# Performance work log

Hardware: AMD Instinct MI355X
Metric: run time of the kernel (lower is better)

The kernel has to match this reference:

```python
import jax, jax.numpy as jnp
import numpy as np

N_EXPERTS = 8
D_MODEL = 1024
D_FF = 4096
BATCH = 4
SEQ = 4096


def setup_inputs() -> dict:
    key = jax.random.key(0)
    k1, k2, k3, k4 = jax.random.split(key, 4)
    hidden_states = jax.random.normal(k1, (BATCH, SEQ, D_MODEL), dtype=jnp.float32)
    expert_indices = jax.random.randint(k2, (BATCH, SEQ), 0, N_EXPERTS, dtype=jnp.int64)
    # Expert MLP params, scaled like standard init
    W1 = jax.random.normal(k3, (N_EXPERTS, D_MODEL, D_FF), dtype=jnp.float32) / np.sqrt(D_MODEL)
    b1 = jnp.zeros((N_EXPERTS, D_FF), dtype=jnp.float32)
    W2 = jax.random.normal(k4, (N_EXPERTS, D_FF, D_MODEL), dtype=jnp.float32) / np.sqrt(D_FF)
    b2 = jnp.zeros((N_EXPERTS, D_MODEL), dtype=jnp.float32)
    return {"hidden_states": hidden_states, "expert_indices": expert_indices,
            "W1": W1, "b1": b1, "W2": W2, "b2": b2}


def reference(hidden_states, expert_indices, W1, b1, W2, b2):
    B, S, D = hidden_states.shape
    flat = hidden_states.reshape(B * S, D)          # [T, D]
    idx = expert_indices.reshape(-1)                 # [T]
    out = jnp.zeros_like(flat)
    # Fixed small loop over experts (structurally distinct weights).
    # jit-friendly: each expert runs over all tokens, output masked per token.
    for e in range(W1.shape[0]):
        h = jax.nn.gelu(flat @ W1[e] + b1[e])        # [T, F]
        y = h @ W2[e] + b2[e]                        # [T, D]
        out = out + jnp.where((idx == e)[:, None], y, jnp.float32(0.0))
    return out.reshape(B, S, D)
```

## Files before the change

kernel.cpp:

```cpp
#include <hip/hip_runtime.h>

#define T_TOK 16384
#define DMODEL 1024
#define DFF 4096
#define NEXP 8
#define BM 128
#define BN 128
#define BK 32
#define LDA 40
#define LDB 40
#define TPAD (T_TOK + NEXP * BM)

#define SEG8 256
#define TP256 (T_TOK + NEXP * SEG8)
#define BM2 256
#define BN2 128
#define BK2 64

typedef __bf16 bf16x8 __attribute__((ext_vector_type(8)));
typedef float f32x4 __attribute__((ext_vector_type(4)));

#define GLOAD16(gp, lp) __builtin_amdgcn_global_load_lds( \
    (const __attribute__((address_space(1))) void*)(gp), \
    (__attribute__((address_space(3))) void*)(lp), 16, 0, 0)

#define MFMA16(a, b, c) __builtin_amdgcn_mfma_f32_16x16x32_bf16(a, b, c, 0, 0, 0)

__device__ __forceinline__ float gelu_f(float x) {
  float u = 0.7978845608028654f * (x + 0.044715f * x * x * x);
  float e = __expf(2.0f * u);
  float th = 1.0f - 2.0f / (e + 1.0f);
  return 0.5f * x * (1.0f + th);
}

__global__ void k_init(int* counts, int* cursors, int* bucket, int n) {
  int i = blockIdx.x * blockDim.x + threadIdx.x;
  if (i < n) bucket[i] = -1;
  if (i < NEXP) { counts[i] = 0; cursors[i] = 0; }
}

__global__ void k_hist(const int* __restrict__ idx, int* counts) {
  int t = blockIdx.x * blockDim.x + threadIdx.x;
  int e = (t < T_TOK) ? idx[t] : -1;
#pragma unroll
  for (int ex = 0; ex < NEXP; ex++) {
    unsigned long long m = __ballot(e == ex);
    if (((threadIdx.x & 63) == 0) && m)
      atomicAdd(&counts[ex], __popcll(m));
  }
}

__global__ void k_scan(const int* __restrict__ counts, int* po, int seg) {
  if (threadIdx.x == 0 && blockIdx.x == 0) {
    int acc = 0;
    for (int e = 0; e < NEXP; e++) {
      po[e] = acc;
      acc += ((counts[e] + seg - 1) / seg) * seg;
    }
    po[NEXP] = acc;
  }
}

__global__ void k_scatter(const int* __restrict__ idx, const int* __restrict__ po,
                          int* cursors, int* bucket) {
  int t = blockIdx.x * blockDim.x + threadIdx.x;
  int lane = threadIdx.x & 63;
  int e = (t < T_TOK) ? idx[t] : -1;
#pragma unroll
  for (int ex = 0; ex < NEXP; ex++) {
    unsigned long long m = __ballot(e == ex);
    if (e == ex) {
      int lead = __ffsll((long long)m) - 1;
      unsigned long long before = m & ((lane == 0) ? 0ull : ((1ull << lane) - 1ull));
      int base = 0;
      if (lane == lead) base = atomicAdd(&cursors[ex], __popcll(m));
      base = __shfl(base, lead);
      bucket[po[ex] + base + __popcll(before)] = t;
    }
  }
}

__global__ __launch_bounds__(256) void k_gather(
    const float* __restrict__ X, const int* __restrict__ bucket,
    __bf16* __restrict__ Xg)
{
  const int r = blockIdx.x;
  const int t = bucket[r];
  const int c = threadIdx.x * 4;
  float4 v = {0.f, 0.f, 0.f, 0.f};
  if (t >= 0) v = *(const float4*)&X[(size_t)t * DMODEL + c];
  union { __bf16 h[4]; uint2 u; } cv;
  cv.h[0] = (__bf16)v.x; cv.h[1] = (__bf16)v.y;
  cv.h[2] = (__bf16)v.z; cv.h[3] = (__bf16)v.w;
  *(uint2*)&Xg[(size_t)r * DMODEL + c] = cv.u;
}

__global__ __launch_bounds__(256) void k_transpose(
    const float* __restrict__ W, __bf16* __restrict__ Wt, int K, int N)
{
  __shared__ float tile[64][65];
  const size_t msz = (size_t)K * N;
  const float* __restrict__ src = W + (size_t)blockIdx.z * msz;
  __bf16* __restrict__ dst = Wt + (size_t)blockIdx.z * msz;
  const int n0 = blockIdx.x * 64, k0 = blockIdx.y * 64;
  const int tc = threadIdx.x & 15, tr = threadIdx.x >> 4;
#pragma unroll
  for (int i = 0; i < 4; i++) {
    float4 v = *(const float4*)&src[(size_t)(k0 + tr + i * 16) * N + n0 + tc * 4];
    tile[tr + i * 16][tc * 4 + 0] = v.x;
    tile[tr + i * 16][tc * 4 + 1] = v.y;
    tile[tr + i * 16][tc * 4 + 2] = v.z;
    tile[tr + i * 16][tc * 4 + 3] = v.w;
  }
  __syncthreads();
#pragma unroll
  for (int i = 0; i < 4; i++) {
    const int n = tr + i * 16;
    union { __bf16 h[4]; uint2 u; } cv;
    cv.h[0] = (__bf16)tile[tc * 4 + 0][n];
    cv.h[1] = (__bf16)tile[tc * 4 + 1][n];
    cv.h[2] = (__bf16)tile[tc * 4 + 2][n];
    cv.h[3] = (__bf16)tile[tc * 4 + 3][n];
    *(uint2*)&dst[(size_t)(n0 + n) * K + k0 + tc * 4] = cv.u;
  }
}

template <int K, int NCT, bool SCATTER>
__global__ __launch_bounds__(512, 4) void k_gemm2p(
    const __bf16* __restrict__ Ag, const __bf16* __restrict__ Wt,
    const float* __restrict__ bias, const int* __restrict__ bucket,
    const int* __restrict__ po, void* __restrict__ outp)
{
  __shared__ __align__(16) __bf16 As[BM2 * BK2];
  __shared__ __align__(16) __bf16 Bs[BN2 * BK2];
  __shared__ int toks[BM2];

  const int tid = threadIdx.x;
  const int b = (int)blockIdx.x;
  const int idx = b >> 3;
  const int row_t = (b & 7) + ((idx / NCT) << 3);
  const int col_t = idx % NCT;
  const int row0 = row_t * BM2;
  if (row0 >= po[NEXP]) return;
  const int nb0 = col_t * BN2;

  int e = 0;
#pragma unroll
  for (int k = 1; k < NEXP; k++) e = (row0 >= po[k]) ? k : e;
  const __bf16* __restrict__ Bw = Wt + (size_t)e * (size_t)(NCT * BN2) * K;

  if constexpr (SCATTER) {
    if (tid < BM2) toks[tid] = bucket[row0 + tid];
  }

  const int wave = tid >> 6;
  const int lane = tid & 63;
  const int wm = (wave >> 1) * 64;
  const int wn = (wave & 1) * 64;
  const int lm = lane & 15;
  const int lq = lane >> 4;

  const int srow = wave * 8 + (lane >> 3);
  const int skq  = (lane & 7) ^ ((lane >> 3) & 7);
  const __bf16* __restrict__ Asrc = Ag + (size_t)(row0 + srow) * K + skq * 8;
  const __bf16* __restrict__ Bsrc = Bw + (size_t)(nb0 + srow) * K + skq * 8;
  __bf16* const Al = As + wave * 512;
  __bf16* const Bl = Bs + wave * 512;

  f32x4 acc[4][4];
#pragma unroll
  for (int i = 0; i < 4; i++)
#pragma unroll
    for (int j = 0; j < 4; j++) acc[i][j] = (f32x4)0.0f;

  const int sA = lm & 7;

  for (int k0 = 0; k0 < K; k0 += BK2) {
    GLOAD16(Asrc + k0,                    Al);
    GLOAD16(Asrc + k0 + (size_t)64 * K,   Al + 4096);
    GLOAD16(Asrc + k0 + (size_t)128 * K,  Al + 8192);
    GLOAD16(Asrc + k0 + (size_t)192 * K,  Al + 12288);
    GLOAD16(Bsrc + k0,                    Bl);
    GLOAD16(Bsrc + k0 + (size_t)64 * K,   Bl + 4096);
    __syncthreads();

#pragma unroll
    for (int h = 0; h < 2; h++) {
      const int ph = (h * 4 + lq) ^ sA;
      bf16x8 af[4], bfr[4];
#pragma unroll
      for (int i = 0; i < 4; i++)
        af[i] = *(const bf16x8*)&As[(wm + i * 16 + lm) * BK2 + ph * 8];
#pragma unroll
      for (int j = 0; j < 4; j++)
        bfr[j] = *(const bf16x8*)&Bs[(wn + j * 16 + lm) * BK2 + ph * 8];
#pragma unroll
      for (int i = 0; i < 4; i++)
#pragma unroll
        for (int j = 0; j < 4; j++)
          acc[i][j] = MFMA16(af[i], bfr[j], acc[i][j]);
    }
    __syncthreads();
  }

  constexpr int N = NCT * BN2;
  const float* __restrict__ bv = bias + (size_t)e * N;
  if constexpr (!SCATTER) {
    __bf16* __restrict__ Hq = (__bf16*)outp;
#pragma unroll
    for (int j = 0; j < 4; j++) {
      const int col = nb0 + wn + j * 16 + lm;
      const float bb = bv[col];
#pragma unroll
      for (int i = 0; i < 4; i++) {
#pragma unroll
        for (int r = 0; r < 4; r++) {
          int row = row0 + wm + i * 16 + lq * 4 + r;
          Hq[(size_t)row * N + col] = (__bf16)gelu_f(acc[i][j][r] + bb);
        }
      }
    }
  } else {
    float* __restrict__ O = (float*)outp;
#pragma unroll
    for (int j = 0; j < 4; j++) {
      const int col = nb0 + wn + j * 16 + lm;
      const float bb = bv[col];
#pragma unroll
      for (int i = 0; i < 4; i++) {
#pragma unroll
        for (int r = 0; r < 4; r++) {
          const int t = toks[wm + i * 16 + lq * 4 + r];
          if (t >= 0) O[(size_t)t * DMODEL + col] = acc[i][j][r] + bb;
        }
      }
    }
  }
}

__global__ __launch_bounds__(256, 2) void k_gemm1b(
    const __bf16* __restrict__ Ag, const __bf16* __restrict__ Wt,
    const float* __restrict__ b1, const int* __restrict__ po,
    __bf16* __restrict__ H)
{
  __shared__ __align__(16) __bf16 As[BM * BK];
  __shared__ __align__(16) __bf16 Bs[BN * BK];
  const int tid = threadIdx.x;
  const int b = (int)blockIdx.x;
  const int slot = b >> 3;
  const int row_t = (b & 7) + ((slot >> 5) << 3);
  const int col_t = slot & 31;
  const int row0 = row_t * BM;
  if (row0 >= po[NEXP]) return;
  const int nb0 = col_t * BN;

  int e = 0;
#pragma unroll
  for (int k = 1; k < NEXP; k++) e = (row0 >= po[k]) ? k : e;
  const __bf16* __restrict__ B = Wt + (size_t)e * DFF * DMODEL;

  f32x4 acc[4][4];
#pragma unroll
  for (int i = 0; i < 4; i++)
#pragma unroll
    for (int j = 0; j < 4; j++) acc[i][j] = (f32x4)0.0f;

  const int wave = tid >> 6;
  const int lane = tid & 63;
  const int wm = (wave & 1) * 64;
  const int wn = (wave >> 1) * 64;
  const int lm = lane & 15;
  const int lq = lane >> 4;

  const int sr = wave * 32 + (lane >> 2);
  const int g  = (lane & 3) ^ ((lane >> 3) & 3);
  const __bf16* Aptr = Ag + (size_t)(row0 + sr) * DMODEL + g * 8;
  const __bf16* Bptr = B + (size_t)(nb0 + sr) * DMODEL + g * 8;
  __bf16* Al = &As[wave * 1024];
  __bf16* Bl = &Bs[wave * 1024];
  const int sA = (lm >> 1) & 3;

  for (int k0 = 0; k0 < DMODEL; k0 += BK) {
    GLOAD16(Aptr + k0, Al);
    GLOAD16(Aptr + k0 + 16 * DMODEL, Al + 512);
    GLOAD16(Bptr + k0, Bl);
    GLOAD16(Bptr + k0 + 16 * DMODEL, Bl + 512);
    __syncthreads();

    bf16x8 af[4], bfr[4];
#pragma unroll
    for (int i = 0; i < 4; i++)
      af[i] = *(const bf16x8*)&As[(wm + i * 16 + lm) * BK + (lq ^ sA) * 8];
#pragma unroll
    for (int j = 0; j < 4; j++)
      bfr[j] = *(const bf16x8*)&Bs[(wn + j * 16 + lm) * BK + (lq ^ sA) * 8];
#pragma unroll
    for (int i = 0; i < 4; i++)
#pragma unroll
      for (int j = 0; j < 4; j++)
        acc[i][j] = __builtin_amdgcn_mfma_f32_16x16x32_bf16(af[i], bfr[j], acc[i][j], 0, 0, 0);
    __syncthreads();
  }

  const float* __restrict__ b1e = b1 + e * DFF;
#pragma unroll
  for (int j = 0; j < 4; j++) {
    const int col = nb0 + wn + j * 16 + lm;
    const float bias = b1e[col];
#pragma unroll
    for (int i = 0; i < 4; i++) {
#pragma unroll
      for (int r = 0; r < 4; r++) {
        int row = row0 + wm + i * 16 + lq * 4 + r;
        H[(size_t)row * DFF + col] = (__bf16)gelu_f(acc[i][j][r] + bias);
      }
    }
  }
}

__global__ __launch_bounds__(256, 2) void k_gemm2b(
    const __bf16* __restrict__ H, const __bf16* __restrict__ Wt,
    const float* __restrict__ b2, const int* __restrict__ bucket,
    const int* __restrict__ po, float* __restrict__ out)
{
  __shared__ __align__(16) __bf16 As[BM * BK];
  __shared__ __align__(16) __bf16 Bs[BN * BK];
  __shared__ int toks[BM];
  const int tid = threadIdx.x;
  const int b = (int)blockIdx.x;
  const int slot = b >> 3;
  const int row_t = (b & 7) + ((slot >> 3) << 3);
  const int col_t = slot & 7;
  const int row0 = row_t * BM;
  if (row0 >= po[NEXP]) return;
  const int nb0 = col_t * BN;

  int e = 0;
#pragma unroll
  for (int k = 1; k < NEXP; k++) e = (row0 >= po[k]) ? k : e;
  const __bf16* __restrict__ B = Wt + (size_t)e * DMODEL * DFF;

  if (tid < BM) toks[tid] = bucket[row0 + tid];

  f32x4 acc[4][4];
#pragma unroll
  for (int i = 0; i < 4; i++)
#pragma unroll
    for (int j = 0; j < 4; j++) acc[i][j] = (f32x4)0.0f;

  const int wave = tid >> 6;
  const int lane = tid & 63;
  const int wm = (wave & 1) * 64;
  const int wn = (wave >> 1) * 64;
  const int lm = lane & 15;
  const int lq = lane >> 4;

  const int sr = wave * 32 + (lane >> 2);
  const int g  = (lane & 3) ^ ((lane >> 3) & 3);
  const __bf16* Aptr = H + (size_t)(row0 + sr) * DFF + g * 8;
  const __bf16* Bptr = B + (size_t)(nb0 + sr) * DFF + g * 8;
  __bf16* Al = &As[wave * 1024];
  __bf16* Bl = &Bs[wave * 1024];
  const int sA = (lm >> 1) & 3;

  for (int k0 = 0; k0 < DFF; k0 += BK) {
    GLOAD16(Aptr + k0, Al);
    GLOAD16(Aptr + k0 + 16 * DFF, Al + 512);
    GLOAD16(Bptr + k0, Bl);
    GLOAD16(Bptr + k0 + 16 * DFF, Bl + 512);
    __syncthreads();

    bf16x8 af[4], bfr[4];
#pragma unroll
    for (int i = 0; i < 4; i++)
      af[i] = *(const bf16x8*)&As[(wm + i * 16 + lm) * BK + (lq ^ sA) * 8];
#pragma unroll
    for (int j = 0; j < 4; j++)
      bfr[j] = *(const bf16x8*)&Bs[(wn + j * 16 + lm) * BK + (lq ^ sA) * 8];
#pragma unroll
    for (int i = 0; i < 4; i++)
#pragma unroll
      for (int j = 0; j < 4; j++)
        acc[i][j] = __builtin_amdgcn_mfma_f32_16x16x32_bf16(af[i], bfr[j], acc[i][j], 0, 0, 0);
    __syncthreads();
  }

  const float* __restrict__ b2e = b2 + e * DMODEL;
#pragma unroll
  for (int j = 0; j < 4; j++) {
    const int col = nb0 + wn + j * 16 + lm;
    const float bias = b2e[col];
#pragma unroll
    for (int i = 0; i < 4; i++) {
#pragma unroll
      for (int r = 0; r < 4; r++) {
        int t = toks[wm + i * 16 + lq * 4 + r];
        if (t >= 0) out[(size_t)t * DMODEL + col] = acc[i][j][r] + bias;
      }
    }
  }
}

__global__ __launch_bounds__(256, 2) void k_gemm1(
    const float* __restrict__ X, const float* __restrict__ W1,
    const float* __restrict__ b1, const int* __restrict__ bucket,
    const int* __restrict__ po, __bf16* __restrict__ H, int base_row)
{
  __shared__ __bf16 As[BM * LDA];
  __shared__ __bf16 Bs[BN * LDB];
  __shared__ int toks[BM];
  const int tid = threadIdx.x;
  const int total = po[NEXP];
  const int row0 = base_row + (int)blockIdx.x * BM;
  if (row0 >= total) return;
  const int nb0 = (int)blockIdx.y * BN;
  int e = 0;
#pragma unroll
  for (int k = 1; k < NEXP; k++) e = (row0 >= po[k]) ? k : e;
  const float* __restrict__ W = W1 + (size_t)e * DMODEL * DFF;
  if (tid < BM) toks[tid] = bucket[row0 + tid];
  __syncthreads();
  f32x4 acc[4][4];
#pragma unroll
  for (int i = 0; i < 4; i++)
#pragma unroll
    for (int j = 0; j < 4; j++) acc[i][j] = (f32x4)0.0f;
  const int wave = tid >> 6, lane = tid & 63;
  const int wm = (wave & 1) * 64, wn = (wave >> 1) * 64;
  const int lm = lane & 15, lq = lane >> 4;
  const int bn = tid & 127, bkh = (tid >> 7) * 16;
  for (int k0 = 0; k0 < DMODEL; k0 += BK) {
#pragma unroll
    for (int i = 0; i < 4; i++) {
      int idx = tid + i * 256;
      int row = idx >> 3, kq = idx & 7;
      int t = toks[row];
      float4 v = {0.f, 0.f, 0.f, 0.f};
      if (t >= 0) v = *(const float4*)(X + (size_t)t * DMODEL + k0 + kq * 4);
      union { __bf16 h[4]; uint2 u; } cv;
      cv.h[0] = (__bf16)v.x; cv.h[1] = (__bf16)v.y;
      cv.h[2] = (__bf16)v.z; cv.h[3] = (__bf16)v.w;
      *(uint2*)&As[row * LDA + kq * 4] = cv.u;
    }
    {
      const float* src = W + (size_t)(k0 + bkh) * DFF + nb0 + bn;
      bf16x8 b0, b1v;
#pragma unroll
      for (int kk = 0; kk < 8; kk++) b0[kk] = (__bf16)src[(size_t)kk * DFF];
#pragma unroll
      for (int kk = 0; kk < 8; kk++) b1v[kk] = (__bf16)src[(size_t)(kk + 8) * DFF];
      *(bf16x8*)&Bs[bn * LDB + bkh] = b0;
      *(bf16x8*)&Bs[bn * LDB + bkh + 8] = b1v;
    }
    __syncthreads();
    bf16x8 af[4], bfr[4];
#pragma unroll
    for (int i = 0; i < 4; i++)
      af[i] = *(const bf16x8*)&As[(wm + i * 16 + lm) * LDA + lq * 8];
#pragma unroll
    for (int j = 0; j < 4; j++)
      bfr[j] = *(const bf16x8*)&Bs[(wn + j * 16 + lm) * LDB + lq * 8];
#pragma unroll
    for (int i = 0; i < 4; i++)
#pragma unroll
      for (int j = 0; j < 4; j++)
        acc[i][j] = __builtin_amdgcn_mfma_f32_16x16x32_bf16(af[i], bfr[j], acc[i][j], 0, 0, 0);
    __syncthreads();
  }
  const float* __restrict__ b1e = b1 + e * DFF;
  const int hbase = (int)blockIdx.x * BM;
#pragma unroll
  for (int j = 0; j < 4; j++) {
    const int col = nb0 + wn + j * 16 + lm;
    const float bias = b1e[col];
#pragma unroll
    for (int i = 0; i < 4; i++)
#pragma unroll
      for (int r = 0; r < 4; r++) {
        int row = hbase + wm + i * 16 + lq * 4 + r;
        H[(size_t)row * DFF + col] = (__bf16)gelu_f(acc[i][j][r] + bias);
      }
  }
}

__global__ __launch_bounds__(256, 2) void k_gemm2(
    const __bf16* __restrict__ H, const float* __restrict__ W2,
    const float* __restrict__ b2, const int* __restrict__ bucket,
    const int* __restrict__ po, float* __restrict__ out, int base_row)
{
  __shared__ __bf16 As[BM * LDA];
  __shared__ __bf16 Bs[BN * LDB];
  __shared__ int toks[BM];
  const int tid = threadIdx.x;
  const int total = po[NEXP];
  const int row0 = base_row + (int)blockIdx.x * BM;
  if (row0 >= total) return;
  const int nb0 = (int)blockIdx.y * BN;
  int e = 0;
#pragma unroll
  for (int k = 1; k < NEXP; k++) e = (row0 >= po[k]) ? k : e;
  const float* __restrict__ W = W2 + (size_t)e * DFF * DMODEL;
  if (tid < BM) toks[tid] = bucket[row0 + tid];
  __syncthreads();
  f32x4 acc[4][4];
#pragma unroll
  for (int i = 0; i < 4; i++)
#pragma unroll
    for (int j = 0; j < 4; j++) acc[i][j] = (f32x4)0.0f;
  const int wave = tid >> 6, lane = tid & 63;
  const int wm = (wave & 1) * 64, wn = (wave >> 1) * 64;
  const int lm = lane & 15, lq = lane >> 4;
  const int bn = tid & 127, bkh = (tid >> 7) * 16;
  const int hbase = (int)blockIdx.x * BM;
  for (int k0 = 0; k0 < DFF; k0 += BK) {
#pragma unroll
    for (int i = 0; i < 2; i++) {
      int idx = tid + i * 256;
      int row = idx >> 2, kq = idx & 3;
      bf16x8 v = *(const bf16x8*)(H + (size_t)(hbase + row) * DFF + k0 + kq * 8);
      *(bf16x8*)&As[row * LDA + kq * 8] = v;
    }
    {
      const float* src = W + (size_t)(k0 + bkh) * DMODEL + nb0 + bn;
      bf16x8 b0, b1v;
#pragma unroll
      for (int kk = 0; kk < 8; kk++) b0[kk] = (__bf16)src[(size_t)kk * DMODEL];
#pragma unroll
      for (int kk = 0; kk < 8; kk++) b1v[kk] = (__bf16)src[(size_t)(kk + 8) * DMODEL];
      *(bf16x8*)&Bs[bn * LDB + bkh] = b0;
      *(bf16x8*)&Bs[bn * LDB + bkh + 8] = b1v;
    }
    __syncthreads();
    bf16x8 af[4], bfr[4];
#pragma unroll
    for (int i = 0; i < 4; i++)
      af[i] = *(const bf16x8*)&As[(wm + i * 16 + lm) * LDA + lq * 8];
#pragma unroll
    for (int j = 0; j < 4; j++)
      bfr[j] = *(const bf16x8*)&Bs[(wn + j * 16 + lm) * LDB + lq * 8];
#pragma unroll
    for (int i = 0; i < 4; i++)
#pragma unroll
      for (int j = 0; j < 4; j++)
        acc[i][j] = __builtin_amdgcn_mfma_f32_16x16x32_bf16(af[i], bfr[j], acc[i][j], 0, 0, 0);
    __syncthreads();
  }
  const float* __restrict__ b2e = b2 + e * DMODEL;
#pragma unroll
  for (int j = 0; j < 4; j++) {
    const int col = nb0 + wn + j * 16 + lm;
    const float bias = b2e[col];
#pragma unroll
    for (int i = 0; i < 4; i++)
#pragma unroll
      for (int r = 0; r < 4; r++) {
        int t = toks[wm + i * 16 + lq * 4 + r];
        if (t >= 0) out[(size_t)t * DMODEL + col] = acc[i][j][r] + bias;
      }
  }
}

__global__ __launch_bounds__(256) void k_fallback(
    const float* __restrict__ X, const int* __restrict__ idx,
    const float* __restrict__ W1, const float* __restrict__ b1,
    const float* __restrict__ W2, const float* __restrict__ b2,
    float* __restrict__ out)
{
  __shared__ float xs[DMODEL];
  __shared__ float hs[DFF];
  const int t = blockIdx.x;
  const int e = idx[t];
  const int tid = threadIdx.x;
  const float* w1 = W1 + (size_t)e * DMODEL * DFF;
  const float* w2 = W2 + (size_t)e * DFF * DMODEL;
  for (int i = tid; i < DMODEL; i += 256) xs[i] = X[(size_t)t * DMODEL + i];
  __syncthreads();
  for (int f = tid; f < DFF; f += 256) {
    float a = 0.f;
    for (int d = 0; d < DMODEL; d++) a += xs[d] * w1[(size_t)d * DFF + f];
    hs[f] = gelu_f(a + b1[e * DFF + f]);
  }
  __syncthreads();
  for (int d = tid; d < DMODEL; d += 256) {
    float a = 0.f;
    for (int f = 0; f < DFF; f++) a += hs[f] * w2[(size_t)f * DMODEL + d];
    out[(size_t)t * DMODEL + d] = a + b2[e * DMODEL + d];
  }
}

extern "C" void kernel_launch(void* const* d_in, const int* in_sizes, int n_in,
                              void* d_out, int out_size, void* d_ws, size_t ws_size,
                              hipStream_t stream) {
  const float* X  = (const float*)d_in[0];
  const int*   EI = (const int*)d_in[1];
  const float* W1 = (const float*)d_in[2];
  const float* b1 = (const float*)d_in[3];
  const float* W2 = (const float*)d_in[4];
  const float* b2 = (const float*)d_in[5];
  float* out = (float*)d_out;

  char* ws = (char*)d_ws;
  int* counts  = (int*)(ws + 0);
  int* cursors = (int*)(ws + 32);
  int* po      = (int*)(ws + 64);
  int* bucket  = (int*)(ws + 512);

  {
    const size_t XG_OFF2 = 512 + (size_t)TP256 * 4;
    const size_t WT_OFF2 = XG_OFF2 + (size_t)TP256 * DMODEL * 2;
    const size_t HF_OFF2 = WT_OFF2 + (size_t)NEXP * DMODEL * DFF * 2;
    const size_t NEED2   = HF_OFF2 + (size_t)TP256 * DFF * 2;
    if (ws_size >= NEED2) {
      __bf16* Xg = (__bf16*)(ws + XG_OFF2);
      __bf16* Wt = (__bf16*)(ws + WT_OFF2);
      __bf16* H  = (__bf16*)(ws + HF_OFF2);

      k_init<<<(TP256 + 255) / 256, 256, 0, stream>>>(counts, cursors, bucket, TP256);
      k_hist<<<(T_TOK + 255) / 256, 256, 0, stream>>>(EI, counts);
      k_scan<<<1, 64, 0, stream>>>(counts, po, SEG8);
      k_scatter<<<(T_TOK + 255) / 256, 256, 0, stream>>>(EI, po, cursors, bucket);
      k_gather<<<TP256, 256, 0, stream>>>(X, bucket, Xg);
      k_transpose<<<dim3(DFF / 64, DMODEL / 64, NEXP), 256, 0, stream>>>(W1, Wt, DMODEL, DFF);
      k_gemm2p<DMODEL, DFF / BN2, false>
          <<<(TP256 / BM2) * (DFF / BN2), 512, 0, stream>>>(Xg, Wt, b1, bucket, po, (void*)H);
      k_transpose<<<dim3(DMODEL / 64, DFF / 64, NEXP), 256, 0, stream>>>(W2, Wt, DFF, DMODEL);
      k_gemm2p<DFF, DMODEL / BN2, true>
          <<<(TP256 / BM2) * (DMODEL / BN2), 512, 0, stream>>>(H, Wt, b2, bucket, po, (void*)out);
      return;
    }
  }

  const int Tpad = TPAD;

  const size_t XG_OFF = 70144;
  const size_t XG_SZ  = (size_t)Tpad * DMODEL * 2;
  const size_t WT_OFF = XG_OFF + XG_SZ;
  const size_t WT_SZ  = (size_t)NEXP * DMODEL * DFF * 2;
  const size_t HF_OFF = WT_OFF + WT_SZ;
  const size_t H_SZ   = (size_t)Tpad * DFF * 2;
  const size_t NEED   = HF_OFF + H_SZ;

  if (ws_size >= NEED) {
    __bf16* Xg = (__bf16*)(ws + XG_OFF);
    __bf16* Wt = (__bf16*)(ws + WT_OFF);
    __bf16* H  = (__bf16*)(ws + HF_OFF);

    k_init<<<(Tpad + 255) / 256, 256, 0, stream>>>(counts, cursors, bucket, Tpad);
    k_hist<<<(T_TOK + 255) / 256, 256, 0, stream>>>(EI, counts);
    k_scan<<<1, 64, 0, stream>>>(counts, po, BM);
    k_scatter<<<(T_TOK + 255) / 256, 256, 0, stream>>>(EI, po, cursors, bucket);
    k_gather<<<Tpad, 256, 0, stream>>>(X, bucket, Xg);
    k_transpose<<<dim3(DFF / 64, DMODEL / 64, NEXP), 256, 0, stream>>>(W1, Wt, DMODEL, DFF);
    k_gemm1b<<<(Tpad / BM) * (DFF / BN), 256, 0, stream>>>(Xg, Wt, b1, po, H);
    k_transpose<<<dim3(DMODEL / 64, DFF / 64, NEXP), 256, 0, stream>>>(W2, Wt, DFF, DMODEL);
    k_gemm2b<<<(Tpad / BM) * (DMODEL / BN), 256, 0, stream>>>(H, Wt, b2, bucket, po, out);
    return;
  }

  const size_t H_OFF = 512 + (size_t)Tpad * 4;
  __bf16* H = (__bf16*)(ws + H_OFF);
  size_t avail = (ws_size > H_OFF) ? ws_size - H_OFF : 0;
  long long crll = (long long)(avail / ((size_t)DFF * 2));
  int CR = (crll > Tpad) ? Tpad : (int)crll;
  CR -= CR % BM;
  if (CR < BM) {
    k_fallback<<<T_TOK, 256, 0, stream>>>(X, EI, W1, b1, W2, b2, out);
    return;
  }
  k_init<<<(Tpad + 255) / 256, 256, 0, stream>>>(counts, cursors, bucket, Tpad);
  k_hist<<<(T_TOK + 255) / 256, 256, 0, stream>>>(EI, counts);
  k_scan<<<1, 64, 0, stream>>>(counts, po, BM);
  k_scatter<<<(T_TOK + 255) / 256, 256, 0, stream>>>(EI, po, cursors, bucket);
  int nchunks = (Tpad + CR - 1) / CR;
  for (int c = 0; c < nchunks; c++) {
    int base = c * CR;
    int rows = Tpad - base; if (rows > CR) rows = CR;
    int mt = rows / BM;
    k_gemm1<<<dim3(mt, DFF / BN), 256, 0, stream>>>(X, W1, b1, bucket, po, H, base);
    k_gemm2<<<dim3(mt, DMODEL / BN), 256, 0, stream>>>(H, W2, b2, bucket, po, out, base);
  }
}
```

Before: 875.4 us.

## Double-buffer GEMM LDS tiles with BK=32 and remap block-to-tile order

Replaces the single-buffered BK=64 GEMM main loop with a two-stage LDS ping-pong at BK=32. Global-to-LDS loads for the next k-tile are issued before the MFMAs on the current one, with one barrier per step. It also changes the LDS swizzle for the narrower tile, raises wave priority around the MFMA block, and remaps block IDs so consecutive blocks share a row tile and spread across columns. The aim is to hide load latency and improve cache reuse, at the cost of twice as many barriers per K and different L2 locality.

```diff
diff --git a/kernel.cpp b/kernel.cpp
--- a/kernel.cpp
+++ b/kernel.cpp
@@ -15,7 +15,7 @@
 #define TP256 (T_TOK + NEXP * SEG8)
 #define BM2 256
 #define BN2 128
-#define BK2 64
+#define BK3 32
 
 typedef __bf16 bf16x8 __attribute__((ext_vector_type(8)));
 typedef float f32x4 __attribute__((ext_vector_type(4)));
@@ -125,21 +125,21 @@
   }
 }
 
-template <int K, int NCT, bool SCATTER>
-__global__ __launch_bounds__(512, 4) void k_gemm2p(
+template <int K, int NCT, int CPX, bool SCATTER>
+__global__ __launch_bounds__(512, 4) void k_gemmdb(
     const __bf16* __restrict__ Ag, const __bf16* __restrict__ Wt,
     const float* __restrict__ bias, const int* __restrict__ bucket,
     const int* __restrict__ po, void* __restrict__ outp)
 {
-  __shared__ __align__(16) __bf16 As[BM2 * BK2];
-  __shared__ __align__(16) __bf16 Bs[BN2 * BK2];
+  __shared__ __align__(16) __bf16 As[2][BM2 * BK3];
+  __shared__ __align__(16) __bf16 Bs[2][BN2 * BK3];
   __shared__ int toks[BM2];
 
   const int tid = threadIdx.x;
   const int b = (int)blockIdx.x;
   const int idx = b >> 3;
-  const int row_t = (b & 7) + ((idx / NCT) << 3);
-  const int col_t = idx % NCT;
+  const int col_t = (b & 7) * CPX + (idx % CPX);
+  const int row_t = idx / CPX;
   const int row0 = row_t * BM2;
   if (row0 >= po[NEXP]) return;
   const int nb0 = col_t * BN2;
@@ -160,12 +160,10 @@
   const int lm = lane & 15;
   const int lq = lane >> 4;
 
-  const int srow = wave * 8 + (lane >> 3);
-  const int skq  = (lane & 7) ^ ((lane >> 3) & 7);
+  const int srow = tid >> 2;
+  const int skq  = (tid & 3) ^ ((tid >> 2) & 3) ^ ((tid >> 4) & 3);
   const __bf16* __restrict__ Asrc = Ag + (size_t)(row0 + srow) * K + skq * 8;
   const __bf16* __restrict__ Bsrc = Bw + (size_t)(nb0 + srow) * K + skq * 8;
-  __bf16* const Al = As + wave * 512;
-  __bf16* const Bl = Bs + wave * 512;
 
   f32x4 acc[4][4];
 #pragma unroll
@@ -173,35 +171,56 @@
 #pragma unroll
     for (int j = 0; j < 4; j++) acc[i][j] = (f32x4)0.0f;
 
-  const int sA = lm & 7;
-
-  for (int k0 = 0; k0 < K; k0 += BK2) {
-    GLOAD16(Asrc + k0,                    Al);
-    GLOAD16(Asrc + k0 + (size_t)64 * K,   Al + 4096);
-    GLOAD16(Asrc + k0 + (size_t)128 * K,  Al + 8192);
-    GLOAD16(Asrc + k0 + (size_t)192 * K,  Al + 12288);
-    GLOAD16(Bsrc + k0,                    Bl);
-    GLOAD16(Bsrc + k0 + (size_t)64 * K,   Bl + 4096);
-    __syncthreads();
-
-#pragma unroll
-    for (int h = 0; h < 2; h++) {
-      const int ph = (h * 4 + lq) ^ sA;
-      bf16x8 af[4], bfr[4];
-#pragma unroll
-      for (int i = 0; i < 4; i++)
-        af[i] = *(const bf16x8*)&As[(wm + i * 16 + lm) * BK2 + ph * 8];
-#pragma unroll
-      for (int j = 0; j < 4; j++)
-        bfr[j] = *(const bf16x8*)&Bs[(wn + j * 16 + lm) * BK2 + ph * 8];
-#pragma unroll
-      for (int i = 0; i < 4; i++)
-#pragma unroll
-        for (int j = 0; j < 4; j++)
-          acc[i][j] = MFMA16(af[i], bfr[j], acc[i][j]);
-    }
-    __syncthreads();
-  }
+  const int ph = lq ^ (lm & 3) ^ ((lm >> 2) & 3);
+
+#define STAGE(S, KT)                                                   \
+  {                                                                    \
+    const size_t ko = (size_t)(KT) * BK3;                              \
+    __bf16* Ab = &As[S][wave * 512];                                   \
+    __bf16* Bb = &Bs[S][wave * 512];                                   \
+    GLOAD16(Asrc + ko, Ab);                                            \
+    GLOAD16(Asrc + ko + (size_t)128 * K, Ab + 4096);                   \
+    GLOAD16(Bsrc + ko, Bb);                                            \
+  }
+
+#define COMPUTE(S)                                                     \
+  {                                                                    \
+    bf16x8 af[4], bfr[4];                                              \
+    _Pragma("unroll")                                                  \
+    for (int i = 0; i < 4; i++)                                        \
+      af[i] = *(const bf16x8*)&As[S][(wm + i * 16 + lm) * BK3 + ph * 8]; \
+    _Pragma("unroll")                                                  \
+    for (int j = 0; j < 4; j++)                                        \
+      bfr[j] = *(const bf16x8*)&Bs[S][(wn + j * 16 + lm) * BK3 + ph * 8]; \
+    __builtin_amdgcn_s_setprio(1);                                     \
+    _Pragma("unroll")                                                  \
+    for (int i = 0; i < 4; i++)                                        \
+      _Pragma("unroll")                                                \
+      for (int j = 0; j < 4; j++)                                      \
+        acc[i][j] = MFMA16(af[i], bfr[j], acc[i][j]);                  \
+    __builtin_amdgcn_s_setprio(0);                                     \
+  }
+
+  constexpr int NT = K / BK3;
+
+  STAGE(0, 0)
+  __syncthreads();
+
+  for (int kt = 0; kt < NT - 2; kt += 2) {
+    STAGE(1, kt + 1)
+    COMPUTE(0)
+    __syncthreads();
+    STAGE(0, kt + 2)
+    COMPUTE(1)
+    __syncthreads();
+  }
+  STAGE(1, NT - 1)
+  COMPUTE(0)
+  __syncthreads();
+  COMPUTE(1)
+
+#undef STAGE
+#undef COMPUTE
 
   constexpr int N = NCT * BN2;
   const float* __restrict__ bv = bias + (size_t)e * N;
@@ -621,10 +640,10 @@
       k_scatter<<<(T_TOK + 255) / 256, 256, 0, stream>>>(EI, po, cursors, bucket);
       k_gather<<<TP256, 256, 0, stream>>>(X, bucket, Xg);
       k_transpose<<<dim3(DFF / 64, DMODEL / 64, NEXP), 256, 0, stream>>>(W1, Wt, DMODEL, DFF);
-      k_gemm2p<DMODEL, DFF / BN2, false>
+      k_gemmdb<DMODEL, DFF / BN2, (DFF / BN2) / 8, false>
           <<<(TP256 / BM2) * (DFF / BN2), 512, 0, stream>>>(Xg, Wt, b1, bucket, po, (void*)H);
       k_transpose<<<dim3(DMODEL / 64, DFF / 64, NEXP), 256, 0, stream>>>(W2, Wt, DFF, DMODEL);
-      k_gemm2p<DFF, DMODEL / BN2, true>
+      k_gemmdb<DFF, DMODEL / BN2, (DMODEL / BN2) / 8, true>
           <<<(TP256 / BM2) * (DMODEL / BN2), 512, 0, stream>>>(H, Wt, b2, bucket, po, (void*)out);
       return;
     }
```

New measurement: 1.010 ms. 15.4% more time.
